# Kernel optimization log

Hardware: AMD Instinct MI355X
Metric: run time of the kernel (lower is better)

Reference implementation:

```python
import jax, jax.numpy as jnp
import numpy as np
from jax import lax

INPUT, HIDDEN, OUT = 5, 32, 2

def setup_inputs() -> dict:
    key = jax.random.key(0)
    ks = jax.random.split(key, 7)
    s_ih = 1.0 / np.sqrt(HIDDEN)
    return {
        "x": jax.random.normal(ks[0], (16384, 200, INPUT), dtype=jnp.float32),
        "W_ih": jax.random.uniform(ks[1], (4 * HIDDEN, INPUT), jnp.float32, -s_ih, s_ih),
        "W_hh": jax.random.uniform(ks[2], (4 * HIDDEN, HIDDEN), jnp.float32, -s_ih, s_ih),
        "b_ih": jax.random.uniform(ks[3], (4 * HIDDEN,), jnp.float32, -s_ih, s_ih),
        "b_hh": jax.random.uniform(ks[4], (4 * HIDDEN,), jnp.float32, -s_ih, s_ih),
        "W_fc": jax.random.uniform(ks[5], (OUT, HIDDEN), jnp.float32, -s_ih, s_ih),
        "b_fc": jax.random.uniform(ks[6], (OUT,), jnp.float32, -s_ih, s_ih),
    }

def reference(x, W_ih, W_hh, b_ih, b_hh, W_fc, b_fc):
    B = x.shape[0]
    # Precompute input projections for all timesteps in one GEMM: [B,T,4H]
    x_proj = jnp.einsum("bti,gi->btg", x, W_ih) + (b_ih + b_hh)
    xs = jnp.swapaxes(x_proj, 0, 1)  # [T, B, 4H]

    def step(carry, xg):
        h, c = carry
        gates = xg + h @ W_hh.T  # [B, 4H]
        i, f, g, o = jnp.split(gates, 4, axis=-1)  # torch gate order i,f,g,o
        i = jax.nn.sigmoid(i)
        f = jax.nn.sigmoid(f)
        g = jnp.tanh(g)
        o = jax.nn.sigmoid(o)
        c = f * c + i * g
        h = o * jnp.tanh(c)
        return (h, c), None

    h0 = jnp.zeros((B, HIDDEN), x.dtype)
    c0 = jnp.zeros((B, HIDDEN), x.dtype)
    (h_n, _), _ = lax.scan(step, (h0, c0), xs)
    return h_n @ W_fc.T + b_fc  # [B, 2]
```

## Files before the change

kernel.cpp:

```cpp
#include <hip/hip_runtime.h>


typedef __bf16 bf16x8 __attribute__((ext_vector_type(8)));
typedef float  f32x4  __attribute__((ext_vector_type(4)));
typedef unsigned int u32;

constexpr int kT = 200, kIN = 5, kH = 32;
constexpr int CT = 40;

union FragU { bf16x8 v; __bf16 b[8]; unsigned short s[8]; u32 u[4]; uint4 q4; };

__device__ __forceinline__ unsigned short bfbits(__bf16 b) {
    union { __bf16 b; unsigned short s; } u; u.b = b; return u.s;
}
__device__ __forceinline__ void split2(float x, __bf16& hi, __bf16& lo) {
    hi = (__bf16)x;
    lo = (__bf16)(x - (float)hi);
}
__device__ __forceinline__ float sigm(float z) {
    return __builtin_amdgcn_rcpf(1.0f + __builtin_amdgcn_exp2f(-1.4426950408889634f * z));
}
__device__ __forceinline__ float tanhv(float z) {
    return fmaf(2.0f,
        __builtin_amdgcn_rcpf(1.0f + __builtin_amdgcn_exp2f(-2.8853900817779268f * z)),
        -1.0f);
}

__global__ __launch_bounds__(64) void lstm_reg(
    const float* __restrict__ x,
    const float* __restrict__ W_ih,
    const float* __restrict__ W_hh,
    const float* __restrict__ b_ih,
    const float* __restrict__ b_hh,
    const float* __restrict__ W_fc,
    const float* __restrict__ b_fc,
    float* __restrict__ out)
{
    __shared__ uint4 xbuf[CT][34];

    const int lane = threadIdx.x;
    const int n16  = lane & 15;
    const int q    = lane >> 4;
    const int b0   = blockIdx.x * 16;

    bf16x8 whhA_h[8], whhA_l[8], wihA[8];
#pragma unroll
    for (int t8 = 0; t8 < 8; ++t8) {
        const int g  = t8 & 3, hb = t8 >> 2;
        const int R  = g * 32 + 8 * (n16 >> 2) + 4 * hb + (n16 & 3);
        FragU H, L;
#pragma unroll
        for (int j = 0; j < 8; ++j)
            split2(W_hh[R * kH + q * 8 + j], H.b[j], L.b[j]);
        whhA_h[t8] = H.v; whhA_l[t8] = L.v;

        float wr[5];
#pragma unroll
        for (int i = 0; i < 5; ++i) wr[i] = W_ih[R * kIN + i];
        __bf16 bh, bl;
        split2(b_ih[R] + b_hh[R], bh, bl);

        FragU F;
        F.u[0] = F.u[1] = F.u[2] = F.u[3] = 0u;
        if (q == 0) {
#pragma unroll
            for (int i = 0; i < 5; ++i) F.b[i] = (__bf16)wr[i];
#pragma unroll
            for (int i = 0; i < 3; ++i) F.b[5 + i] = (__bf16)wr[i];
        } else if (q == 1) {
            F.b[0] = (__bf16)wr[3];
            F.b[1] = (__bf16)wr[4];
#pragma unroll
            for (int i = 0; i < 5; ++i) {
                __bf16 hbb, lbb; split2(wr[i], hbb, lbb);
                F.b[2 + i] = lbb;
            }
            F.b[7] = bh;
        } else if (q == 2) {
            F.b[0] = bl;
        }
        wihA[t8] = F.v;
    }

    for (int t2 = lane; t2 < CT; t2 += 64) {
        xbuf[t2][32] = make_uint4(0x3F80u, 0u, 0u, 0u);
        xbuf[t2][33] = make_uint4(0u, 0u, 0u, 0u);
    }

    const int col = (q < 2) ? (n16 * 2 + q) : (30 + q);
    const f32x4 zf4 = {0.f, 0.f, 0.f, 0.f};

    float c8[8] = {0.f, 0.f, 0.f, 0.f, 0.f, 0.f, 0.f, 0.f};
    float hf[8] = {0.f, 0.f, 0.f, 0.f, 0.f, 0.f, 0.f, 0.f};
    FragU Bh, Bl;
    Bh.u[0] = Bh.u[1] = Bh.u[2] = Bh.u[3] = 0u;
    Bl.u[0] = Bl.u[1] = Bl.u[2] = Bl.u[3] = 0u;

    f32x4 xn[8];

    for (int phase = 0; phase < kT / CT; ++phase) {
        {
            const int mm = lane >> 2, pp = lane & 3;
            const float2* xr2 = (const float2*)(x + (size_t)(b0 + mm) * (kT * kIN)
                                                  + (size_t)(phase * CT + pp * 10) * kIN);
            float xv[50];
#pragma unroll
            for (int i = 0; i < 25; ++i) {
                float2 v = xr2[i];
                xv[2 * i] = v.x; xv[2 * i + 1] = v.y;
            }
#pragma unroll
            for (int s5 = 0; s5 < 10; ++s5) {
                u32 xh[5], xl[5];
#pragma unroll
                for (int i = 0; i < 5; ++i) {
                    __bf16 hbb, lbb; split2(xv[s5 * 5 + i], hbb, lbb);
                    xh[i] = bfbits(hbb); xl[i] = bfbits(lbb);
                }
                uint4 f0 = make_uint4(xh[0] | (xh[1] << 16),
                                      xh[2] | (xh[3] << 16),
                                      xh[4] | (xl[0] << 16),
                                      xl[1] | (xl[2] << 16));
                uint4 f1 = make_uint4(xl[3] | (xl[4] << 16),
                                      xh[0] | (xh[1] << 16),
                                      xh[2] | (xh[3] << 16),
                                      xh[4] | (0x3F80u << 16));
                const int tc = pp * 10 + s5;
                xbuf[tc][mm * 2 + 0] = f0;
                xbuf[tc][mm * 2 + 1] = f1;
            }
        }
        __syncthreads();

        {
            FragU xg; xg.q4 = xbuf[0][col];
#pragma unroll
            for (int t8 = 0; t8 < 8; ++t8)
                xn[t8] = __builtin_amdgcn_mfma_f32_16x16x32_bf16(wihA[t8], xg.v, zf4, 0, 0, 0);
        }

#pragma unroll 1
        for (int tc = 0; tc < CT; ++tc) {
            f32x4 acc[8];
#pragma unroll
            for (int t8 = 0; t8 < 8; ++t8) {
                f32x4 a = __builtin_amdgcn_mfma_f32_16x16x32_bf16(whhA_h[t8], Bh.v, xn[t8], 0, 0, 0);
                a = __builtin_amdgcn_mfma_f32_16x16x32_bf16(whhA_h[t8], Bl.v, a, 0, 0, 0);
                a = __builtin_amdgcn_mfma_f32_16x16x32_bf16(whhA_l[t8], Bh.v, a, 0, 0, 0);
                acc[t8] = a;
            }

            {
                const int tn = (tc + 1 < CT) ? tc + 1 : 0;
                FragU xg; xg.q4 = xbuf[tn][col];
#pragma unroll
                for (int t8 = 0; t8 < 8; ++t8)
                    xn[t8] = __builtin_amdgcn_mfma_f32_16x16x32_bf16(wihA[t8], xg.v, zf4, 0, 0, 0);
            }

#pragma unroll
            for (int jj = 0; jj < 8; ++jj) {
                const int hb = jj >> 2, r = jj & 3;
                float iv = sigm (acc[hb * 4 + 0][r]);
                float fv = sigm (acc[hb * 4 + 1][r]);
                float gv = tanhv(acc[hb * 4 + 2][r]);
                float ov = sigm (acc[hb * 4 + 3][r]);
                float cn = fmaf(fv, c8[jj], iv * gv);
                c8[jj] = cn;
                float hn = ov * tanhv(cn);
                hf[jj] = hn;
                split2(hn, Bh.b[jj], Bl.b[jj]);
            }
        }
    }

    float* hfin = (float*)xbuf;
    __syncthreads();
#pragma unroll
    for (int jj = 0; jj < 8; ++jj)
        hfin[n16 * 33 + q * 8 + jj] = hf[jj];
    __syncthreads();
    if (lane < 32) {
        const int m = lane >> 1, o = lane & 1;
        float s = b_fc[o];
#pragma unroll
        for (int j = 0; j < kH; ++j)
            s = fmaf(hfin[m * 33 + j], W_fc[o * kH + j], s);
        out[(size_t)(b0 + m) * 2 + o] = s;
    }
}

extern "C" void kernel_launch(void* const* d_in, const int* in_sizes, int n_in,
                              void* d_out, int out_size, void* d_ws, size_t ws_size,
                              hipStream_t stream) {
    const float* x    = (const float*)d_in[0];
    const float* W_ih = (const float*)d_in[1];
    const float* W_hh = (const float*)d_in[2];
    const float* b_ih = (const float*)d_in[3];
    const float* b_hh = (const float*)d_in[4];
    const float* W_fc = (const float*)d_in[5];
    const float* b_fc = (const float*)d_in[6];
    float* out = (float*)d_out;

    hipLaunchKernelGGL(lstm_reg, dim3(1024), dim3(64), 0, stream,
                       x, W_ih, W_hh, b_ih, b_hh, W_fc, b_fc, out);
}
```

Measured before the change: 275.1 us.

## Halve batch per wave to 8 and split gate nonlinearity work across lane halves

```diff
diff --git a/kernel.cpp b/kernel.cpp
--- a/kernel.cpp
+++ b/kernel.cpp
@@ -26,7 +26,7 @@
         -1.0f);
 }
 
-__global__ __launch_bounds__(64) void lstm_reg(
+__global__ __launch_bounds__(64) void lstm_reg2(
     const float* __restrict__ x,
     const float* __restrict__ W_ih,
     const float* __restrict__ W_hh,
@@ -36,12 +36,14 @@
     const float* __restrict__ b_fc,
     float* __restrict__ out)
 {
-    __shared__ uint4 xbuf[CT][34];
+    __shared__ uint4 xbuf[CT][18];
 
     const int lane = threadIdx.x;
     const int n16  = lane & 15;
     const int q    = lane >> 4;
-    const int b0   = blockIdx.x * 16;
+    const int half = n16 >> 3;
+    const int bb   = n16 & 7;
+    const int b0   = blockIdx.x * 8;
 
     bf16x8 whhA_h[8], whhA_l[8], wihA[8];
 #pragma unroll
@@ -83,15 +85,15 @@
     }
 
     for (int t2 = lane; t2 < CT; t2 += 64) {
-        xbuf[t2][32] = make_uint4(0x3F80u, 0u, 0u, 0u);
-        xbuf[t2][33] = make_uint4(0u, 0u, 0u, 0u);
-    }
-
-    const int col = (q < 2) ? (n16 * 2 + q) : (30 + q);
+        xbuf[t2][16] = make_uint4(0x3F80u, 0u, 0u, 0u);
+        xbuf[t2][17] = make_uint4(0u, 0u, 0u, 0u);
+    }
+
+    const int col = (q < 2) ? (bb * 2 + q) : (14 + q);
     const f32x4 zf4 = {0.f, 0.f, 0.f, 0.f};
 
-    float c8[8] = {0.f, 0.f, 0.f, 0.f, 0.f, 0.f, 0.f, 0.f};
-    float hf[8] = {0.f, 0.f, 0.f, 0.f, 0.f, 0.f, 0.f, 0.f};
+    float c4s[4] = {0.f, 0.f, 0.f, 0.f};
+    float hf[4]  = {0.f, 0.f, 0.f, 0.f};
     FragU Bh, Bl;
     Bh.u[0] = Bh.u[1] = Bh.u[2] = Bh.u[3] = 0u;
     Bl.u[0] = Bl.u[1] = Bl.u[2] = Bl.u[3] = 0u;
@@ -100,17 +102,14 @@
 
     for (int phase = 0; phase < kT / CT; ++phase) {
         {
-            const int mm = lane >> 2, pp = lane & 3;
-            const float2* xr2 = (const float2*)(x + (size_t)(b0 + mm) * (kT * kIN)
-                                                  + (size_t)(phase * CT + pp * 10) * kIN);
-            float xv[50];
-#pragma unroll
-            for (int i = 0; i < 25; ++i) {
-                float2 v = xr2[i];
-                xv[2 * i] = v.x; xv[2 * i + 1] = v.y;
-            }
-#pragma unroll
-            for (int s5 = 0; s5 < 10; ++s5) {
+            const int mm = lane >> 3, pp = lane & 7;
+            const float* xrow = x + (size_t)(b0 + mm) * (kT * kIN)
+                                  + (size_t)(phase * CT + pp * 5) * kIN;
+            float xv[25];
+#pragma unroll
+            for (int i = 0; i < 25; ++i) xv[i] = xrow[i];
+#pragma unroll
+            for (int s5 = 0; s5 < 5; ++s5) {
                 u32 xh[5], xl[5];
 #pragma unroll
                 for (int i = 0; i < 5; ++i) {
@@ -125,7 +124,7 @@
                                       xh[0] | (xh[1] << 16),
                                       xh[2] | (xh[3] << 16),
                                       xh[4] | (0x3F80u << 16));
-                const int tc = pp * 10 + s5;
+                const int tc = pp * 5 + s5;
                 xbuf[tc][mm * 2 + 0] = f0;
                 xbuf[tc][mm * 2 + 1] = f1;
             }
@@ -158,29 +157,49 @@
                     xn[t8] = __builtin_amdgcn_mfma_f32_16x16x32_bf16(wihA[t8], xg.v, zf4, 0, 0, 0);
             }
 
-#pragma unroll
-            for (int jj = 0; jj < 8; ++jj) {
-                const int hb = jj >> 2, r = jj & 3;
-                float iv = sigm (acc[hb * 4 + 0][r]);
-                float fv = sigm (acc[hb * 4 + 1][r]);
-                float gv = tanhv(acc[hb * 4 + 2][r]);
-                float ov = sigm (acc[hb * 4 + 3][r]);
-                float cn = fmaf(fv, c8[jj], iv * gv);
-                c8[jj] = cn;
+            f32x4 av[4];
+#pragma unroll
+            for (int g = 0; g < 4; ++g) av[g] = half ? acc[4 + g] : acc[g];
+
+            u32 ph[4], pl[4];
+#pragma unroll
+            for (int r = 0; r < 4; ++r) {
+                float iv = sigm (av[0][r]);
+                float fv = sigm (av[1][r]);
+                float gv = tanhv(av[2][r]);
+                float ov = sigm (av[3][r]);
+                float cn = fmaf(fv, c4s[r], iv * gv);
+                c4s[r] = cn;
                 float hn = ov * tanhv(cn);
-                hf[jj] = hn;
-                split2(hn, Bh.b[jj], Bl.b[jj]);
-            }
-        }
-    }
-
+                hf[r] = hn;
+                __bf16 hh, hl;
+                split2(hn, hh, hl);
+                ph[r] = bfbits(hh); pl[r] = bfbits(hl);
+            }
+            u32 oh0 = ph[0] | (ph[1] << 16), oh1 = ph[2] | (ph[3] << 16);
+            u32 ol0 = pl[0] | (pl[1] << 16), ol1 = pl[2] | (pl[3] << 16);
+            u32 sh0 = (u32)__shfl_xor((int)oh0, 8);
+            u32 sh1 = (u32)__shfl_xor((int)oh1, 8);
+            u32 sl0 = (u32)__shfl_xor((int)ol0, 8);
+            u32 sl1 = (u32)__shfl_xor((int)ol1, 8);
+            Bh.u[0] = half ? sh0 : oh0;
+            Bh.u[1] = half ? sh1 : oh1;
+            Bh.u[2] = half ? oh0 : sh0;
+            Bh.u[3] = half ? oh1 : sh1;
+            Bl.u[0] = half ? sl0 : ol0;
+            Bl.u[1] = half ? sl1 : ol1;
+            Bl.u[2] = half ? ol0 : sl0;
+            Bl.u[3] = half ? ol1 : sl1;
+        }
+    }
+
+    __syncthreads();
     float* hfin = (float*)xbuf;
+#pragma unroll
+    for (int r = 0; r < 4; ++r)
+        hfin[bb * 33 + q * 8 + 4 * half + r] = hf[r];
     __syncthreads();
-#pragma unroll
-    for (int jj = 0; jj < 8; ++jj)
-        hfin[n16 * 33 + q * 8 + jj] = hf[jj];
-    __syncthreads();
-    if (lane < 32) {
+    if (lane < 16) {
         const int m = lane >> 1, o = lane & 1;
         float s = b_fc[o];
 #pragma unroll
@@ -202,6 +221,6 @@
     const float* b_fc = (const float*)d_in[6];
     float* out = (float*)d_out;
 
-    hipLaunchKernelGGL(lstm_reg, dim3(1024), dim3(64), 0, stream,
+    hipLaunchKernelGGL(lstm_reg2, dim3(2048), dim3(64), 0, stream,
                        x, W_ih, W_hh, b_ih, b_hh, W_fc, b_fc, out);
 }
```

After: 637.1 us. 132% more time.

## Fold log2e scaling into weights and share reciprocals across paired LSTM cells

Applied to the files above, without the earlier changes.

```diff
diff --git a/kernel.cpp b/kernel.cpp
--- a/kernel.cpp
+++ b/kernel.cpp
@@ -8,6 +8,9 @@
 constexpr int kT = 200, kIN = 5, kH = 32;
 constexpr int CT = 40;
 
+constexpr float kL  = 1.4426950408889634f;
+constexpr float k2L = 2.8853900817779268f;
+
 union FragU { bf16x8 v; __bf16 b[8]; unsigned short s[8]; u32 u[4]; uint4 q4; };
 
 __device__ __forceinline__ unsigned short bfbits(__bf16 b) {
@@ -17,16 +20,8 @@
     hi = (__bf16)x;
     lo = (__bf16)(x - (float)hi);
 }
-__device__ __forceinline__ float sigm(float z) {
-    return __builtin_amdgcn_rcpf(1.0f + __builtin_amdgcn_exp2f(-1.4426950408889634f * z));
-}
-__device__ __forceinline__ float tanhv(float z) {
-    return fmaf(2.0f,
-        __builtin_amdgcn_rcpf(1.0f + __builtin_amdgcn_exp2f(-2.8853900817779268f * z)),
-        -1.0f);
-}
-
-__global__ __launch_bounds__(64) void lstm_reg(
+
+__global__ __launch_bounds__(64) void lstm_reg5(
     const float* __restrict__ x,
     const float* __restrict__ W_ih,
     const float* __restrict__ W_hh,
@@ -48,17 +43,18 @@
     for (int t8 = 0; t8 < 8; ++t8) {
         const int g  = t8 & 3, hb = t8 >> 2;
         const int R  = g * 32 + 8 * (n16 >> 2) + 4 * hb + (n16 & 3);
+        const float sc = (g == 2) ? k2L : kL;
         FragU H, L;
 #pragma unroll
         for (int j = 0; j < 8; ++j)
-            split2(W_hh[R * kH + q * 8 + j], H.b[j], L.b[j]);
+            split2(sc * W_hh[R * kH + q * 8 + j], H.b[j], L.b[j]);
         whhA_h[t8] = H.v; whhA_l[t8] = L.v;
 
         float wr[5];
 #pragma unroll
-        for (int i = 0; i < 5; ++i) wr[i] = W_ih[R * kIN + i];
+        for (int i = 0; i < 5; ++i) wr[i] = sc * W_ih[R * kIN + i];
         __bf16 bh, bl;
-        split2(b_ih[R] + b_hh[R], bh, bl);
+        split2(sc * (b_ih[R] + b_hh[R]), bh, bl);
 
         FragU F;
         F.u[0] = F.u[1] = F.u[2] = F.u[3] = 0u;
@@ -91,12 +87,9 @@
     const f32x4 zf4 = {0.f, 0.f, 0.f, 0.f};
 
     float c8[8] = {0.f, 0.f, 0.f, 0.f, 0.f, 0.f, 0.f, 0.f};
-    float hf[8] = {0.f, 0.f, 0.f, 0.f, 0.f, 0.f, 0.f, 0.f};
     FragU Bh, Bl;
     Bh.u[0] = Bh.u[1] = Bh.u[2] = Bh.u[3] = 0u;
     Bl.u[0] = Bl.u[1] = Bl.u[2] = Bl.u[3] = 0u;
-
-    f32x4 xn[8];
 
     for (int phase = 0; phase < kT / CT; ++phase) {
         {
@@ -132,53 +125,74 @@
         }
         __syncthreads();
 
-        {
-            FragU xg; xg.q4 = xbuf[0][col];
-#pragma unroll
-            for (int t8 = 0; t8 < 8; ++t8)
-                xn[t8] = __builtin_amdgcn_mfma_f32_16x16x32_bf16(wihA[t8], xg.v, zf4, 0, 0, 0);
-        }
+        FragU xg; xg.q4 = xbuf[0][col];
 
 #pragma unroll 1
         for (int tc = 0; tc < CT; ++tc) {
+            FragU xgn;
+            const int tn = (tc + 1 < CT) ? tc + 1 : 0;
+            xgn.q4 = xbuf[tn][col];
+
             f32x4 acc[8];
 #pragma unroll
             for (int t8 = 0; t8 < 8; ++t8) {
-                f32x4 a = __builtin_amdgcn_mfma_f32_16x16x32_bf16(whhA_h[t8], Bh.v, xn[t8], 0, 0, 0);
+                f32x4 a = __builtin_amdgcn_mfma_f32_16x16x32_bf16(wihA[t8], xg.v, zf4, 0, 0, 0);
+                a = __builtin_amdgcn_mfma_f32_16x16x32_bf16(whhA_h[t8], Bh.v, a, 0, 0, 0);
                 a = __builtin_amdgcn_mfma_f32_16x16x32_bf16(whhA_h[t8], Bl.v, a, 0, 0, 0);
                 a = __builtin_amdgcn_mfma_f32_16x16x32_bf16(whhA_l[t8], Bh.v, a, 0, 0, 0);
                 acc[t8] = a;
             }
 
-            {
-                const int tn = (tc + 1 < CT) ? tc + 1 : 0;
-                FragU xg; xg.q4 = xbuf[tn][col];
-#pragma unroll
-                for (int t8 = 0; t8 < 8; ++t8)
-                    xn[t8] = __builtin_amdgcn_mfma_f32_16x16x32_bf16(wihA[t8], xg.v, zf4, 0, 0, 0);
-            }
-
-#pragma unroll
-            for (int jj = 0; jj < 8; ++jj) {
-                const int hb = jj >> 2, r = jj & 3;
-                float iv = sigm (acc[hb * 4 + 0][r]);
-                float fv = sigm (acc[hb * 4 + 1][r]);
-                float gv = tanhv(acc[hb * 4 + 2][r]);
-                float ov = sigm (acc[hb * 4 + 3][r]);
-                float cn = fmaf(fv, c8[jj], iv * gv);
-                c8[jj] = cn;
-                float hn = ov * tanhv(cn);
-                hf[jj] = hn;
-                split2(hn, Bh.b[jj], Bl.b[jj]);
-            }
+#pragma unroll
+            for (int m2 = 0; m2 < 4; ++m2) {
+                const int j0 = 2 * m2, j1 = j0 + 1;
+                const int hb = j0 >> 2;
+                const int r0 = j0 & 3, r1 = j1 & 3;
+                float ai0 = acc[hb * 4 + 0][r0], af0 = acc[hb * 4 + 1][r0];
+                float ag0 = acc[hb * 4 + 2][r0], ao0 = acc[hb * 4 + 3][r0];
+                float ai1 = acc[hb * 4 + 0][r1], af1 = acc[hb * 4 + 1][r1];
+                float ag1 = acc[hb * 4 + 2][r1], ao1 = acc[hb * 4 + 3][r1];
+
+                float u0 = __builtin_amdgcn_exp2f(-ai0), v0 = __builtin_amdgcn_exp2f(-ag0);
+                float w0 = __builtin_amdgcn_exp2f(-af0), p0 = __builtin_amdgcn_exp2f(-ao0);
+                float u1 = __builtin_amdgcn_exp2f(-ai1), v1 = __builtin_amdgcn_exp2f(-ag1);
+                float w1 = __builtin_amdgcn_exp2f(-af1), p1 = __builtin_amdgcn_exp2f(-ao1);
+
+                float A0 = (1.0f + u0) * (1.0f + v0);
+                float A1 = (1.0f + u1) * (1.0f + v1);
+                float B0 = 1.0f + w0, B1 = 1.0f + w1;
+                float rA = __builtin_amdgcn_rcpf(A0 * A1);
+                float rB = __builtin_amdgcn_rcpf(B0 * B1);
+
+                float t0 = fmaf(v0, -k2L, k2L);
+                float t1 = fmaf(v1, -k2L, k2L);
+                float c0 = fmaf(c8[j0], B1 * rB, t0 * (A1 * rA));
+                float c1 = fmaf(c8[j1], B0 * rB, t1 * (A0 * rA));
+                c0 = fmaxf(c0, -35.0f);
+                c1 = fmaxf(c1, -35.0f);
+                c8[j0] = c0; c8[j1] = c1;
+
+                float s0 = __builtin_amdgcn_exp2f(-c0);
+                float s1 = __builtin_amdgcn_exp2f(-c1);
+                float C0 = (1.0f + p0) * (1.0f + s0);
+                float C1 = (1.0f + p1) * (1.0f + s1);
+                float rC = __builtin_amdgcn_rcpf(C0 * C1);
+                float h0 = (1.0f - s0) * (C1 * rC);
+                float h1 = (1.0f - s1) * (C0 * rC);
+
+                split2(h0, Bh.b[j0], Bl.b[j0]);
+                split2(h1, Bh.b[j1], Bl.b[j1]);
+            }
+
+            xg = xgn;
         }
     }
 
+    __syncthreads();
     float* hfin = (float*)xbuf;
-    __syncthreads();
 #pragma unroll
     for (int jj = 0; jj < 8; ++jj)
-        hfin[n16 * 33 + q * 8 + jj] = hf[jj];
+        hfin[n16 * 33 + q * 8 + jj] = (float)Bh.b[jj] + (float)Bl.b[jj];
     __syncthreads();
     if (lane < 32) {
         const int m = lane >> 1, o = lane & 1;
@@ -202,6 +216,6 @@
     const float* b_fc = (const float*)d_in[6];
     float* out = (float*)d_out;
 
-    hipLaunchKernelGGL(lstm_reg, dim3(1024), dim3(64), 0, stream,
+    hipLaunchKernelGGL(lstm_reg5, dim3(1024), dim3(64), 0, stream,
                        x, W_ih, W_hh, b_ih, b_hh, W_fc, b_fc, out);
 }
```

Result: faster. 243.9 us (-11.3%).
